# Performance work log

Hardware: AMD Instinct MI355X
Metric: run time of the kernel (lower is better)

The kernel has to match this reference:

```python
import jax, jax.numpy as jnp
import numpy as np
from jax import lax

L_LAYERS = 8
HID = 300


def _reverse_padded(x, lengths):
    # x: [T, B, D]; reverse each sequence within its valid length, keep padding zero.
    T = x.shape[0]
    t = jnp.arange(T)[:, None]                      # [T,1]
    rev = lengths[None, :] - 1 - t                  # [T,B]
    valid = (rev >= 0)
    idx = jnp.clip(rev, 0, T - 1)
    g = jnp.take_along_axis(x, idx[:, :, None].astype(jnp.int32), axis=0)
    return g * valid[:, :, None].astype(x.dtype)


def _run_layer(x, W_ih, W_hh, b, lengths, reverse):
    # x: [T,B,D] time-major. W_ih: [D,6H], W_hh: [H,5H], b: [5H]
    T, B, _ = x.shape
    H = W_hh.shape[0]
    if reverse:
        x = _reverse_padded(x, lengths)
    pi = jnp.einsum('tbd,dg->tbg', x, W_ih)         # [T,B,6H] input projections
    mask = (jnp.arange(T)[:, None] < lengths[None, :])[:, :, None]  # [T,B,1] bool

    def step(carry, xt):
        h, c = carry
        pi_t, m = xt
        ps = h @ W_hh + b                            # [B,5H]
        z = pi_t[:, :5 * H] + ps                     # fused pre-activations
        i = jax.nn.sigmoid(z[:, 0 * H:1 * H])
        f = jax.nn.sigmoid(z[:, 1 * H:2 * H])
        g = jnp.tanh(z[:, 2 * H:3 * H])
        o = jax.nn.sigmoid(z[:, 3 * H:4 * H])
        r = jax.nn.sigmoid(z[:, 4 * H:5 * H])        # highway gate
        c_new = i * g + f * c
        lstm_out = o * jnp.tanh(c_new)
        h_new = r * lstm_out + (1.0 - r) * pi_t[:, 5 * H:]  # highway connection
        c = jnp.where(m, c_new, c)
        h = jnp.where(m, h_new, h)
        return (h, c), h_new * m.astype(h_new.dtype)

    init = (jnp.zeros((B, H), x.dtype), jnp.zeros((B, H), x.dtype))
    (_, _), ys = lax.scan(step, init, (pi, mask))
    if reverse:
        ys = _reverse_padded(ys, lengths)
    return ys


def setup_inputs() -> dict:
    key = jax.random.key(0)
    ks = jax.random.split(key, 6)
    B, T, D = 64, 256, 200
    inputs = jax.random.normal(ks[0], (B, T, D), dtype=jnp.float32)
    lengths = jnp.sort(jax.random.randint(ks[1], (B,), 1, T + 1))[::-1].astype(jnp.int32)
    s = 0.08
    W_ih0 = jax.random.normal(ks[2], (D, 6 * HID), dtype=jnp.float32) * s
    W_ih_rest = jax.random.normal(ks[3], (L_LAYERS - 1, HID, 6 * HID), dtype=jnp.float32) * s
    W_hh = jax.random.normal(ks[4], (L_LAYERS, HID, 5 * HID), dtype=jnp.float32) * s
    b_hh = jnp.zeros((L_LAYERS, 5 * HID), dtype=jnp.float32)
    b_hh = b_hh.at[:, HID:2 * HID].set(1.0)  # forget-gate bias init to 1
    return {"inputs": inputs, "lengths": lengths, "W_ih0": W_ih0,
            "W_ih_rest": W_ih_rest, "W_hh": W_hh, "b_hh": b_hh}


def reference(inputs, lengths, W_ih0, W_ih_rest, W_hh, b_hh):
    # inputs: [B,T,D] batch-first -> time-major [T,B,D]
    x = jnp.transpose(inputs, (1, 0, 2))
    per_layer = []
    for layer in range(L_LAYERS):
        Wih = W_ih0 if layer == 0 else W_ih_rest[layer - 1]
        x = _run_layer(x, Wih, W_hh[layer], b_hh[layer], lengths, reverse=(layer % 2 == 1))
        per_layer.append(x)
    hidden = jnp.stack(per_layer)                    # [L,T,B,H] (matches hy[:,1:])
    output = jnp.transpose(x, (1, 0, 2))             # [B,T,H], zero past lengths
    return output, hidden
```

## Files before the change

### kernel.cpp

```cpp
#include <hip/hip_runtime.h>
#include <hip/hip_bf16.h>

#define B_ 64
#define T_ 256
#define D_ 200
#define H_ 300
#define L_ 8
#define M_ 16384
#define NG 1800
#define NZ 1500
#define KP 320
#define NBP 2048

typedef __attribute__((ext_vector_type(8))) short bf16x8;
typedef __attribute__((ext_vector_type(4))) float f32x4;
typedef __attribute__((ext_vector_type(4))) unsigned u32x4;
typedef unsigned long long ull;

__device__ __forceinline__ unsigned short f2bf(float f) {
  union { float f; unsigned u; } v; v.f = f;
  unsigned r = v.u + 0x7fffu + ((v.u >> 16) & 1u);
  return (unsigned short)(r >> 16);
}

__device__ __forceinline__ float sigf(float x) { return 1.f / (1.f + __expf(-x)); }
__device__ __forceinline__ float tanhf_(float x) {
  x = fminf(15.f, fmaxf(-15.f, x));
  float e = __expf(2.f * x);
  return (e - 1.f) / (e + 1.f);
}

#define BARRIER() asm volatile("s_waitcnt lgkmcnt(0)\n\ts_barrier" ::: "memory")

__device__ __forceinline__ u32x4 ld128_nt(const ull* p) {
  u32x4 v;
  asm volatile("global_load_dwordx4 %0, %1, off nt\n\ts_waitcnt vmcnt(0)"
               : "=v"(v) : "v"(p) : "memory");
  return v;
}
__device__ __forceinline__ u32x4 ld128_sys(const ull* p) {
  u32x4 v;
  asm volatile("global_load_dwordx4 %0, %1, off sc0 sc1\n\ts_waitcnt vmcnt(0)"
               : "=v"(v) : "v"(p) : "memory");
  return v;
}
__device__ __forceinline__ int ld32_nt(const int* p) {
  int v;
  asm volatile("global_load_dword %0, %1, off nt\n\ts_waitcnt vmcnt(0)"
               : "=v"(v) : "v"(p) : "memory");
  return v;
}
__device__ __forceinline__ void st64_plain(ull* p, ull v) {
  asm volatile("global_store_dwordx2 %0, %1, off" :: "v"(p), "v"(v) : "memory");
}
__device__ __forceinline__ void st64_sys(ull* p, ull v) {
  asm volatile("global_store_dwordx2 %0, %1, off sc0 sc1" :: "v"(p), "v"(v) : "memory");
}

__device__ __forceinline__ void gl_lds16(const unsigned short* g, unsigned short* l) {
  __builtin_amdgcn_global_load_lds(
      (const __attribute__((address_space(1))) void*)g,
      (__attribute__((address_space(3))) void*)l, 16, 0, 0);
}

__global__ void k_transpose_w(const float* __restrict__ W0, const float* __restrict__ Wr,
                              unsigned short* __restrict__ WbT) {
  __shared__ unsigned short t_lds[64][65];
  const int n0 = blockIdx.x * 64;
  const int k0 = blockIdx.y * 64;
  const int l = blockIdx.z;
  const int Kl = (l == 0) ? D_ : H_;
  const float* W = (l == 0) ? W0 : (Wr + (size_t)(l - 1) * H_ * NG);
  unsigned short* out = WbT + (size_t)l * NBP * KP;
  const int tx = threadIdx.x & 63;
  const int ty = threadIdx.x >> 6;
  #pragma unroll
  for (int i = 0; i < 16; i++) {
    int k = k0 + ty * 16 + i;
    int n = n0 + tx;
    float v = (k < Kl && n < NG) ? W[(size_t)k * NG + n] : 0.f;
    t_lds[ty * 16 + i][tx] = f2bf(v);
  }
  __syncthreads();
  #pragma unroll
  for (int i = 0; i < 16; i++) {
    int n = n0 + ty * 16 + i;
    if (n < NG) out[(size_t)n * KP + k0 + tx] = t_lds[tx][ty * 16 + i];
  }
}

__global__ void k_transpose_in(const float* __restrict__ inp, unsigned short* __restrict__ xb) {
  int i = blockIdx.x * blockDim.x + threadIdx.x;
  if (i >= T_ * B_ * D_) return;
  int d = i % D_;
  int r = i / D_;
  int b = r % B_;
  int t = r / B_;
  xb[(size_t)r * KP + d] = f2bf(inp[((size_t)b * T_ + t) * D_ + d]);
}

__global__ void k_out(const float* __restrict__ hid7, float* __restrict__ outp) {
  int i = blockIdx.x * blockDim.x + threadIdx.x;
  if (i >= B_ * T_ * H_) return;
  int j = i % H_;
  int r = i / H_;
  int t = r % T_;
  int b = r / T_;
  outp[i] = hid7[((size_t)t * B_ + b) * H_ + j];
}

__global__ __launch_bounds__(256) void k_gemm(const unsigned short* __restrict__ A,
                                              const unsigned short* __restrict__ Bt,
                                              float* __restrict__ C, int nk) {
  __shared__ unsigned short As[128 * 32];
  __shared__ unsigned short Bs[128 * 32];
  const int bm = blockIdx.x, bn = blockIdx.y;
  const int tid = threadIdx.x;
  const int lane = tid & 63, wid = tid >> 6;
  const int wm = wid & 1, wn = wid >> 1;
  const int l16 = lane & 15, quad = lane >> 4;
  const int srow = lane >> 2;
  const int sswz = ((lane & 3) ^ (srow & 3)) << 3;
  const int sA = ((quad ^ (l16 & 3)) << 3);
  const size_t arow0 = (size_t)bm * 128;
  const size_t brow0 = (size_t)bn * 128;
  f32x4 acc[4][4] = {};
  for (int kc = 0; kc < nk; kc++) {
    const int k0 = kc << 5;
    #pragma unroll
    for (int r = 0; r < 2; r++) {
      const int rbase = r * 64 + wid * 16;
      gl_lds16(A  + (arow0 + rbase + srow) * KP + k0 + sswz, &As[rbase * 32]);
      gl_lds16(Bt + (brow0 + rbase + srow) * KP + k0 + sswz, &Bs[rbase * 32]);
    }
    asm volatile("s_waitcnt vmcnt(0)" ::: "memory");
    __syncthreads();
    bf16x8 af[4], bfr[4];
    #pragma unroll
    for (int i = 0; i < 4; i++) {
      af[i]  = *(const bf16x8*)&As[(wm * 64 + i * 16 + l16) * 32 + sA];
      bfr[i] = *(const bf16x8*)&Bs[(wn * 64 + i * 16 + l16) * 32 + sA];
    }
    #pragma unroll
    for (int mi = 0; mi < 4; mi++)
      #pragma unroll
      for (int ni = 0; ni < 4; ni++)
        acc[mi][ni] = __builtin_amdgcn_mfma_f32_16x16x32_bf16(af[mi], bfr[ni], acc[mi][ni], 0, 0, 0);
    __syncthreads();
  }
  const int row0 = bm * 128 + wm * 64 + quad * 4;
  const int col0 = bn * 128 + wn * 64 + l16;
  #pragma unroll
  for (int mi = 0; mi < 4; mi++) {
    #pragma unroll
    for (int ni = 0; ni < 4; ni++) {
      int col = col0 + ni * 16;
      if (col < NG) {
        #pragma unroll
        for (int i = 0; i < 4; i++)
          C[(size_t)(row0 + mi * 16 + i) * NG + col] = acc[mi][ni][i];
      }
    }
  }
}

struct PiR { float v0, v1, v2, v3, v4, v6; };

__device__ __forceinline__ void pi_pref_row(PiR& r, const float* __restrict__ pi,
                                            int lr, int rev, int ss, int br, int j2) {
  r.v0 = r.v1 = r.v2 = r.v3 = r.v4 = r.v6 = 0.f;
  if (ss < lr) {
    int t = rev ? (lr - 1 - ss) : ss;
    const float* pr = pi + ((size_t)t * B_ + br) * NG;
    r.v0 = pr[j2]; r.v1 = pr[300 + j2]; r.v2 = pr[600 + j2];
    r.v3 = pr[900 + j2]; r.v4 = pr[1200 + j2]; r.v6 = pr[NZ + j2];
  }
}

__device__ __forceinline__ void poll_stash(unsigned tg, int par, int pt,
                                           const ull* hwf, const ull* hws,
                                           unsigned short* h_lds) {
  const ull* pf = hwf + par + 2 * pt;
  const ull* ps = hws + par + 2 * pt;
  u32x4 v;
  int miss = 0;
  for (;;) {
    v = ld128_nt(pf);
    if ((v.y == tg) && (v.w == tg)) break;
    if ((++miss & 31) == 0) {
      v = ld128_sys(ps);
      if ((v.y == tg) && (v.w == tg)) break;
      __builtin_amdgcn_s_sleep(1);
    }
  }
  int w0 = pt << 1;
  int r2 = (w0 >= 300) ? 1 : 0;
  int k = w0 - r2 * 300;
  h_lds[(2 * r2) * 328 + k]     = (unsigned short)(v.x >> 16);
  h_lds[(2 * r2 + 1) * 328 + k] = (unsigned short)(v.x & 0xffffu);
  int w1 = w0 + 1;
  int r2b = (w1 >= 300) ? 1 : 0;
  int kb = w1 - r2b * 300;
  h_lds[(2 * r2b) * 328 + kb]     = (unsigned short)(v.z >> 16);
  h_lds[(2 * r2b + 1) * 328 + kb] = (unsigned short)(v.z & 0xffffu);
}

__global__ __launch_bounds__(512, 2) void k_fused(
    float* __restrict__ pi, const float* __restrict__ Whh,
    const float* __restrict__ bias, const int* __restrict__ lens,
    float* __restrict__ hid, unsigned short* __restrict__ xb,
    ull* __restrict__ h_words, int* __restrict__ prog,
    const unsigned short* __restrict__ Bt_next, int rev, int tagbase)
{
  const int bid = blockIdx.x;
  const int tid = threadIdx.x;

  if (bid < 192) {
    __shared__ __align__(16) unsigned short h_lds[16 * 328];
    __shared__ __align__(16) float z_lds[128 * 4];
    __shared__ float bias_s[128];
    __shared__ int len_s[4];

    const int g = bid & 15;
    const int cb = bid >> 4;

    const int lane = tid & 63;
    const int wid = tid >> 6;
    const int l16 = lane & 15;
    const int quad = lane >> 4;

    const int rp = tid / 25;
    const int gj = tid - rp * 25;
    const int j2 = cb * 25 + gj;

    bf16x8 wfrag[10];
    {
      int n = wid * 16 + l16;
      bool vn = n < 125;
      int colw = vn ? ((n / 25) * 300 + cb * 25 + (n % 25)) : 0;
      #pragma unroll
      for (int c = 0; c < 10; c++) {
        bf16x8 f;
        #pragma unroll
        for (int j = 0; j < 8; j++) {
          int k = c * 32 + quad * 8 + j;
          float v = (vn && k < 300) ? Whh[(size_t)k * NZ + colw] : 0.f;
          f[j] = (short)f2bf(v);
        }
        wfrag[c] = f;
      }
    }
    if (tid < 4) len_s[tid] = lens[g * 4 + tid];
    if (tid < 125) bias_s[tid] = bias[(tid / 25) * 300 + cb * 25 + (tid % 25)];
    for (int i = tid; i < 16 * 328; i += 512) h_lds[i] = 0;
    __syncthreads();

    int S = len_s[0];
    S = len_s[1] > S ? len_s[1] : S;
    S = len_s[2] > S ? len_s[2] : S;
    S = len_s[3] > S ? len_s[3] : S;

    ull* hwf = h_words + (size_t)g * 1200;
    ull* hws = h_words + 16 * 1200 + (size_t)g * 1200;
    const int brbase = g * 4;
    float cA = 0.f, cB = 0.f;

    PiR pa, pb;
    int lA = 0, lB = 0;
    if (tid < 50) {
      lA = len_s[2 * rp]; lB = len_s[2 * rp + 1];
      pi_pref_row(pa, pi, lA, rev, 0, brbase + 2 * rp,     j2);
      pi_pref_row(pb, pi, lB, rev, 0, brbase + 2 * rp + 1, j2);
    }

    for (int s = 0; s < S; s++) {
      if (s > 0 && tid >= 64 && tid < 364)
        poll_stash((unsigned)(tagbase + s), (s & 1) * 600, tid - 64, hwf, hws, h_lds);
      BARRIER();

      f32x4 acc = {0, 0, 0, 0};
      if (s > 0) {
        f32x4 acc2 = {0, 0, 0, 0};
        const unsigned short* abase = &h_lds[l16 * 328 + quad * 8];
        #pragma unroll
        for (int c = 0; c < 10; c += 2) {
          bf16x8 a0 = *(const bf16x8*)(abase + c * 32);
          bf16x8 a1 = *(const bf16x8*)(abase + c * 32 + 32);
          acc  = __builtin_amdgcn_mfma_f32_16x16x32_bf16(a0, wfrag[c],     acc,  0, 0, 0);
          acc2 = __builtin_amdgcn_mfma_f32_16x16x32_bf16(a1, wfrag[c + 1], acc2, 0, 0, 0);
        }
        acc += acc2;
      }
      if (quad == 0) {
        int n = wid * 16 + l16;
        *(f32x4*)&z_lds[n * 4] = acc;
      }
      BARRIER();

      if (tid < 50) {
        asm volatile("s_waitcnt vmcnt(0)" ::: "memory");
        const float bb0 = bias_s[gj],      bb1 = bias_s[25 + gj], bb2 = bias_s[50 + gj];
        const float bb3 = bias_s[75 + gj], bb4 = bias_s[100 + gj];
        const float2 z0 = *(const float2*)&z_lds[(gj      ) * 4 + 2 * rp];
        const float2 z1 = *(const float2*)&z_lds[(25 + gj ) * 4 + 2 * rp];
        const float2 z2 = *(const float2*)&z_lds[(50 + gj ) * 4 + 2 * rp];
        const float2 z3 = *(const float2*)&z_lds[(75 + gj ) * 4 + 2 * rp];
        const float2 z4 = *(const float2*)&z_lds[(100 + gj) * 4 + 2 * rp];
        float iA = sigf(z0.x + pa.v0 + bb0);
        float fA = sigf(z1.x + pa.v1 + bb1);
        float gA = tanhf_(z2.x + pa.v2 + bb2);
        float oA = sigf(z3.x + pa.v3 + bb3);
        float rA = sigf(z4.x + pa.v4 + bb4);
        float cnA = iA * gA + fA * cA; cA = cnA;
        float hA = rA * (oA * tanhf_(cnA)) + (1.f - rA) * pa.v6;
        float iB = sigf(z0.y + pb.v0 + bb0);
        float fB = sigf(z1.y + pb.v1 + bb1);
        float gB = tanhf_(z2.y + pb.v2 + bb2);
        float oB = sigf(z3.y + pb.v3 + bb3);
        float rB = sigf(z4.y + pb.v4 + bb4);
        float cnB = iB * gB + fB * cB; cB = cnB;
        float hB = rB * (oB * tanhf_(cnB)) + (1.f - rB) * pb.v6;

        unsigned short hbA = f2bf(hA), hbB = f2bf(hB);
        ull word = ((ull)(unsigned)(tagbase + s + 1) << 32)
                 | ((unsigned)hbA << 16) | (unsigned)hbB;
        int pidx = ((s + 1) & 1) * 600 + rp * 300 + j2;
        st64_plain(hwf + pidx, word);
        st64_sys(hws + pidx, word);
        if (tid == 0) prog[g * 12 + cb] = tagbase + s + 1;
        if (s < lA) {
          int t = rev ? (lA - 1 - s) : s;
          int br = brbase + 2 * rp;
          hid[((size_t)t * B_ + br) * H_ + j2] = hA;
          xb[((size_t)t * B_ + br) * KP + j2] = hbA;
        }
        if (s < lB) {
          int t = rev ? (lB - 1 - s) : s;
          int br = brbase + 2 * rp + 1;
          hid[((size_t)t * B_ + br) * H_ + j2] = hB;
          xb[((size_t)t * B_ + br) * KP + j2] = hbB;
        }
        pi_pref_row(pa, pi, lA, rev, s + 1, brbase + 2 * rp,     j2);
        pi_pref_row(pb, pi, lB, rev, s + 1, brbase + 2 * rp + 1, j2);
      }
    }
    if (tid < 64) {
      asm volatile("s_waitcnt vmcnt(0)" ::: "memory");
      if (tid == 0) prog[g * 12 + cb] = tagbase + 299;
    }
  } else {
    __shared__ unsigned short As[128 * 32];
    __shared__ unsigned short Bs2[2][128 * 32];
    const int w = bid - 192;
    const int cls = w & 7;
    const int k8 = w >> 3;
    const int g = (k8 < 4) ? cls : cls + 8;
    const int q = k8 & 3;
    const int lane = tid & 63;
    const int wid = tid >> 6;
    const int wg = tid >> 8;
    const int w4 = wid & 3;
    const int l16 = lane & 15, quad = lane >> 4;
    const int srow = lane >> 2;
    const int sswz = ((lane & 3) ^ (srow & 3)) << 3;
    const int sA = ((quad ^ (l16 & 3)) << 3);
    const int wm = w4 & 1, wn = w4 >> 1;
    const int Sg = lens[4 * g];

    for (int ci = 0; ci < 8; ci++) {
      const int chunk = rev ? (7 - ci) : ci;
      const int t0 = chunk * 32;
      int need = rev ? (Sg - t0 + 1) : (t0 + 33);
      if (t0 >= Sg) need = 0;
      if (need > 0) {
        if (tid == 0) {
          const int target = tagbase + need;
          for (;;) {
            int mn = 0x7fffffff;
            for (int cbx = 0; cbx < 12; cbx++) {
              int v = ld32_nt(prog + g * 12 + cbx);
              mn = v < mn ? v : mn;
            }
            if (mn >= target) break;
            __builtin_amdgcn_s_sleep(8);
          }
        }
        __syncthreads();
      }
      #pragma unroll 1
      for (int cpi = 0; cpi < 2; cpi++) {
        const int cp = 2 * q + cpi;
        const unsigned short* BtB = Bt_next + (size_t)(cp * 256 + wg * 128) * KP;
        f32x4 acc[4][4] = {};
        for (int kc = 0; kc < 10; kc++) {
          const int k0 = kc << 5;
          {
            int rl = wid * 16 + srow;
            int xrow = (t0 + (rl >> 2)) * 64 + g * 4 + (rl & 3);
            gl_lds16(xb + (size_t)xrow * KP + k0 + sswz, &As[(wid * 16) * 32]);
          }
          #pragma unroll
          for (int r = 0; r < 2; r++) {
            int rbase = w4 * 32 + r * 16;
            gl_lds16(BtB + (size_t)(rbase + srow) * KP + k0 + sswz, &Bs2[wg][rbase * 32]);
          }
          asm volatile("s_waitcnt vmcnt(0)" ::: "memory");
          __syncthreads();
          bf16x8 af[4], bfr[4];
          #pragma unroll
          for (int i = 0; i < 4; i++) {
            af[i]  = *(const bf16x8*)&As[(wm * 64 + i * 16 + l16) * 32 + sA];
            bfr[i] = *(const bf16x8*)&Bs2[wg][(wn * 64 + i * 16 + l16) * 32 + sA];
          }
          #pragma unroll
          for (int mi = 0; mi < 4; mi++)
            #pragma unroll
            for (int ni = 0; ni < 4; ni++)
              acc[mi][ni] = __builtin_amdgcn_mfma_f32_16x16x32_bf16(af[mi], bfr[ni], acc[mi][ni], 0, 0, 0);
          __syncthreads();
        }
        #pragma unroll
        for (int mi = 0; mi < 4; mi++) {
          #pragma unroll
          for (int ni = 0; ni < 4; ni++) {
            int col = cp * 256 + wg * 128 + wn * 64 + ni * 16 + l16;
            if (col < NG) {
              #pragma unroll
              for (int i = 0; i < 4; i++) {
                int rl = wm * 64 + mi * 16 + quad * 4 + i;
                int prow = (t0 + (rl >> 2)) * 64 + g * 4 + (rl & 3);
                pi[(size_t)prow * NG + col] = acc[mi][ni][i];
              }
            }
          }
        }
      }
    }
  }
}

extern "C" void kernel_launch(void* const* d_in, const int* in_sizes, int n_in,
                              void* d_out, int out_size, void* d_ws, size_t ws_size,
                              hipStream_t stream) {
  const float* inputs = (const float*)d_in[0];
  const int* lengths = (const int*)d_in[1];
  const float* W_ih0 = (const float*)d_in[2];
  const float* W_ih_rest = (const float*)d_in[3];
  const float* W_hh = (const float*)d_in[4];
  const float* b_hh = (const float*)d_in[5];
  float* outp = (float*)d_out;
  float* hidden = outp + (size_t)B_ * T_ * H_;

  char* ws = (char*)d_ws;
  float* pi = (float*)ws;
  size_t off = (size_t)M_ * NG * 4;
  unsigned short* xb = (unsigned short*)(ws + off);
  off += (size_t)M_ * KP * 2;
  unsigned short* WbT = (unsigned short*)(ws + off);
  off += (size_t)L_ * NBP * KP * 2;
  ull* h_words = (ull*)(ws + off);
  size_t hw_bytes = 32ull * 1200 * 8 + 16 * 12 * 4;
  int* prog = (int*)(ws + off + 32ull * 1200 * 8);
  off += hw_bytes;

  hipMemsetAsync(d_out, 0, (size_t)out_size * 4, stream);
  hipMemsetAsync(h_words, 0, hw_bytes, stream);
  hipMemsetAsync(xb, 0, (size_t)M_ * KP * 2, stream);
  hipMemsetAsync(WbT, 0, (size_t)L_ * NBP * KP * 2, stream);

  k_transpose_w<<<dim3(29, 5, 8), 256, 0, stream>>>(W_ih0, W_ih_rest, WbT);
  {
    int n = T_ * B_ * D_;
    k_transpose_in<<<(n + 255) / 256, 256, 0, stream>>>(inputs, xb);
  }
  k_gemm<<<dim3(M_ / 128, 15), 256, 0, stream>>>(xb, WbT, pi, 7);
  for (int l = 0; l < L_; l++) {
    float* hid_l = hidden + (size_t)l * T_ * B_ * H_;
    const unsigned short* Bt_next = WbT + (size_t)(l + 1) * NBP * KP;
    int grid = (l < L_ - 1) ? 256 : 192;
    k_fused<<<grid, 512, 0, stream>>>(pi, W_hh + (size_t)l * H_ * NZ, b_hh + (size_t)l * NZ,
                                      lengths, hid_l, xb, h_words, prog,
                                      Bt_next, l & 1, l * 300);
  }
  k_out<<<((B_ * T_ * H_) + 255) / 256, 256, 0, stream>>>(
      hidden + (size_t)(L_ - 1) * T_ * B_ * H_, outp);
}
```

Measured before the change: 3.326 ms.

## Poll per-group epoch counters before reading tagged hidden words

Replaces per-thread polling on tagged hidden-state words with a wave-level ballot over 12 per-column-block epoch counters. Producers publish an epoch after their hidden stores drain, through both plain and system-scope stores. The old tag-polling loop stays as a fallback. Also splits the recurrent MFMA chain into four accumulators, drops the s>0 guard, and raises wave priority in the gate/activation section. The extra waitcnt before publishing the epoch adds latency on the critical path, and correctness now depends on the epoch store becoming visible after the data stores.

```diff
diff --git a/kernel.cpp b/kernel.cpp
--- a/kernel.cpp
+++ b/kernel.cpp
@@ -50,11 +50,23 @@
                : "=v"(v) : "v"(p) : "memory");
   return v;
 }
+__device__ __forceinline__ int ld32_sys_i(const int* p) {
+  int v;
+  asm volatile("global_load_dword %0, %1, off sc0 sc1\n\ts_waitcnt vmcnt(0)"
+               : "=v"(v) : "v"(p) : "memory");
+  return v;
+}
 __device__ __forceinline__ void st64_plain(ull* p, ull v) {
   asm volatile("global_store_dwordx2 %0, %1, off" :: "v"(p), "v"(v) : "memory");
 }
 __device__ __forceinline__ void st64_sys(ull* p, ull v) {
   asm volatile("global_store_dwordx2 %0, %1, off sc0 sc1" :: "v"(p), "v"(v) : "memory");
+}
+__device__ __forceinline__ void st32_plain(int* p, int v) {
+  asm volatile("global_store_dword %0, %1, off" :: "v"(p), "v"(v) : "memory");
+}
+__device__ __forceinline__ void st32_sys_i(int* p, int v) {
+  asm volatile("global_store_dword %0, %1, off sc0 sc1" :: "v"(p), "v"(v) : "memory");
 }
 
 __device__ __forceinline__ void gl_lds16(const unsigned short* g, unsigned short* l) {
@@ -177,39 +189,11 @@
   }
 }
 
-__device__ __forceinline__ void poll_stash(unsigned tg, int par, int pt,
-                                           const ull* hwf, const ull* hws,
-                                           unsigned short* h_lds) {
-  const ull* pf = hwf + par + 2 * pt;
-  const ull* ps = hws + par + 2 * pt;
-  u32x4 v;
-  int miss = 0;
-  for (;;) {
-    v = ld128_nt(pf);
-    if ((v.y == tg) && (v.w == tg)) break;
-    if ((++miss & 31) == 0) {
-      v = ld128_sys(ps);
-      if ((v.y == tg) && (v.w == tg)) break;
-      __builtin_amdgcn_s_sleep(1);
-    }
-  }
-  int w0 = pt << 1;
-  int r2 = (w0 >= 300) ? 1 : 0;
-  int k = w0 - r2 * 300;
-  h_lds[(2 * r2) * 328 + k]     = (unsigned short)(v.x >> 16);
-  h_lds[(2 * r2 + 1) * 328 + k] = (unsigned short)(v.x & 0xffffu);
-  int w1 = w0 + 1;
-  int r2b = (w1 >= 300) ? 1 : 0;
-  int kb = w1 - r2b * 300;
-  h_lds[(2 * r2b) * 328 + kb]     = (unsigned short)(v.z >> 16);
-  h_lds[(2 * r2b + 1) * 328 + kb] = (unsigned short)(v.z & 0xffffu);
-}
-
 __global__ __launch_bounds__(512, 2) void k_fused(
     float* __restrict__ pi, const float* __restrict__ Whh,
     const float* __restrict__ bias, const int* __restrict__ lens,
     float* __restrict__ hid, unsigned short* __restrict__ xb,
-    ull* __restrict__ h_words, int* __restrict__ prog,
+    ull* __restrict__ h_words, int* __restrict__ ep_pl, int* __restrict__ ep_sy,
     const unsigned short* __restrict__ Bt_next, int rev, int tagbase)
 {
   const int bid = blockIdx.x;
@@ -262,6 +246,8 @@
 
     ull* hwf = h_words + (size_t)g * 1200;
     ull* hws = h_words + 16 * 1200 + (size_t)g * 1200;
+    int* epl = ep_pl + g * 16;
+    int* eps = ep_sy + g * 16;
     const int brbase = g * 4;
     float cA = 0.f, cB = 0.f;
 
@@ -274,31 +260,74 @@
     }
 
     for (int s = 0; s < S; s++) {
-      if (s > 0 && tid >= 64 && tid < 364)
-        poll_stash((unsigned)(tagbase + s), (s & 1) * 600, tid - 64, hwf, hws, h_lds);
+      if (s > 0 && tid >= 64 && tid < 364) {
+        const unsigned tg = (unsigned)(tagbase + s);
+        const int par = (s & 1) * 600;
+        const int pt = tid - 64;
+        const ull* pf = hwf + par + 2 * pt;
+        const ull* ps = hws + par + 2 * pt;
+        u32x4 v;
+        bool ok = false;
+        for (int it = 0; it < 64; ++it) {
+          int e = (lane < 12) ? ld32_nt(epl + lane) : 0x7fffffff;
+          ull bal = __ballot(e >= (int)tg);
+          if ((bal & 0xFFFull) == 0xFFFull) { ok = true; break; }
+        }
+        if (ok) {
+          v = ld128_nt(pf);
+          ok = (v.y == tg) && (v.w == tg);
+        }
+        if (!ok) {
+          int miss = 0;
+          for (;;) {
+            v = ld128_nt(pf);
+            if ((v.y == tg) && (v.w == tg)) break;
+            if ((++miss & 31) == 0) {
+              v = ld128_sys(ps);
+              if ((v.y == tg) && (v.w == tg)) break;
+              __builtin_amdgcn_s_sleep(1);
+            }
+          }
+        }
+        int w0 = pt << 1;
+        int r2 = (w0 >= 300) ? 1 : 0;
+        int k = w0 - r2 * 300;
+        h_lds[(2 * r2) * 328 + k]     = (unsigned short)(v.x >> 16);
+        h_lds[(2 * r2 + 1) * 328 + k] = (unsigned short)(v.x & 0xffffu);
+        int w1 = w0 + 1;
+        int r2b = (w1 >= 300) ? 1 : 0;
+        int kb = w1 - r2b * 300;
+        h_lds[(2 * r2b) * 328 + kb]     = (unsigned short)(v.z >> 16);
+        h_lds[(2 * r2b + 1) * 328 + kb] = (unsigned short)(v.z & 0xffffu);
+      }
       BARRIER();
 
-      f32x4 acc = {0, 0, 0, 0};
-      if (s > 0) {
-        f32x4 acc2 = {0, 0, 0, 0};
+      {
+        f32x4 a0 = {0,0,0,0}, a1 = {0,0,0,0}, a2 = {0,0,0,0}, a3 = {0,0,0,0};
         const unsigned short* abase = &h_lds[l16 * 328 + quad * 8];
         #pragma unroll
-        for (int c = 0; c < 10; c += 2) {
-          bf16x8 a0 = *(const bf16x8*)(abase + c * 32);
-          bf16x8 a1 = *(const bf16x8*)(abase + c * 32 + 32);
-          acc  = __builtin_amdgcn_mfma_f32_16x16x32_bf16(a0, wfrag[c],     acc,  0, 0, 0);
-          acc2 = __builtin_amdgcn_mfma_f32_16x16x32_bf16(a1, wfrag[c + 1], acc2, 0, 0, 0);
-        }
-        acc += acc2;
-      }
-      if (quad == 0) {
-        int n = wid * 16 + l16;
-        *(f32x4*)&z_lds[n * 4] = acc;
+        for (int c = 0; c < 10; c += 4) {
+          bf16x8 h0 = *(const bf16x8*)(abase + c * 32);
+          bf16x8 h1 = *(const bf16x8*)(abase + c * 32 + 32);
+          a0 = __builtin_amdgcn_mfma_f32_16x16x32_bf16(h0, wfrag[c],     a0, 0, 0, 0);
+          a1 = __builtin_amdgcn_mfma_f32_16x16x32_bf16(h1, wfrag[c + 1], a1, 0, 0, 0);
+          if (c + 2 < 10) {
+            bf16x8 h2 = *(const bf16x8*)(abase + c * 32 + 64);
+            bf16x8 h3 = *(const bf16x8*)(abase + c * 32 + 96);
+            a2 = __builtin_amdgcn_mfma_f32_16x16x32_bf16(h2, wfrag[c + 2], a2, 0, 0, 0);
+            a3 = __builtin_amdgcn_mfma_f32_16x16x32_bf16(h3, wfrag[c + 3], a3, 0, 0, 0);
+          }
+        }
+        f32x4 acc = (a0 + a1) + (a2 + a3);
+        if (quad == 0) {
+          int n = wid * 16 + l16;
+          *(f32x4*)&z_lds[n * 4] = acc;
+        }
       }
       BARRIER();
 
       if (tid < 50) {
-        asm volatile("s_waitcnt vmcnt(0)" ::: "memory");
+        __builtin_amdgcn_s_setprio(1);
         const float bb0 = bias_s[gj],      bb1 = bias_s[25 + gj], bb2 = bias_s[50 + gj];
         const float bb3 = bias_s[75 + gj], bb4 = bias_s[100 + gj];
         const float2 z0 = *(const float2*)&z_lds[(gj      ) * 4 + 2 * rp];
@@ -326,8 +355,12 @@
                  | ((unsigned)hbA << 16) | (unsigned)hbB;
         int pidx = ((s + 1) & 1) * 600 + rp * 300 + j2;
         st64_plain(hwf + pidx, word);
+        asm volatile("s_waitcnt vmcnt(0)" ::: "memory");
+        if (tid == 0) {
+          st32_plain(epl + cb, tagbase + s + 1);
+          st32_sys_i(eps + cb, tagbase + s + 1);
+        }
         st64_sys(hws + pidx, word);
-        if (tid == 0) prog[g * 12 + cb] = tagbase + s + 1;
         if (s < lA) {
           int t = rev ? (lA - 1 - s) : s;
           int br = brbase + 2 * rp;
@@ -342,11 +375,13 @@
         }
         pi_pref_row(pa, pi, lA, rev, s + 1, brbase + 2 * rp,     j2);
         pi_pref_row(pb, pi, lB, rev, s + 1, brbase + 2 * rp + 1, j2);
-      }
-    }
-    if (tid < 64) {
+        __builtin_amdgcn_s_setprio(0);
+      }
+    }
+    if (tid == 0) {
       asm volatile("s_waitcnt vmcnt(0)" ::: "memory");
-      if (tid == 0) prog[g * 12 + cb] = tagbase + 299;
+      st32_plain(epl + cb, tagbase + 299);
+      st32_sys_i(eps + cb, tagbase + 299);
     }
   } else {
     __shared__ unsigned short As[128 * 32];
@@ -375,13 +410,16 @@
       if (need > 0) {
         if (tid == 0) {
           const int target = tagbase + need;
+          int iters = 0;
           for (;;) {
             int mn = 0x7fffffff;
             for (int cbx = 0; cbx < 12; cbx++) {
-              int v = ld32_nt(prog + g * 12 + cbx);
+              int v = (iters < 256) ? ld32_nt(ep_pl + g * 16 + cbx)
+                                    : ld32_sys_i(ep_sy + g * 16 + cbx);
               mn = v < mn ? v : mn;
             }
             if (mn >= target) break;
+            iters++;
             __builtin_amdgcn_s_sleep(8);
           }
         }
@@ -459,8 +497,10 @@
   unsigned short* WbT = (unsigned short*)(ws + off);
   off += (size_t)L_ * NBP * KP * 2;
   ull* h_words = (ull*)(ws + off);
-  size_t hw_bytes = 32ull * 1200 * 8 + 16 * 12 * 4;
-  int* prog = (int*)(ws + off + 32ull * 1200 * 8);
+  size_t data_bytes = 32ull * 1200 * 8;
+  int* ep_pl = (int*)(ws + off + data_bytes);
+  int* ep_sy = ep_pl + 16 * 16;
+  size_t hw_bytes = data_bytes + 2ull * 16 * 16 * 4;
   off += hw_bytes;
 
   hipMemsetAsync(d_out, 0, (size_t)out_size * 4, stream);
@@ -479,7 +519,7 @@
     const unsigned short* Bt_next = WbT + (size_t)(l + 1) * NBP * KP;
     int grid = (l < L_ - 1) ? 256 : 192;
     k_fused<<<grid, 512, 0, stream>>>(pi, W_hh + (size_t)l * H_ * NZ, b_hh + (size_t)l * NZ,
-                                      lengths, hid_l, xb, h_words, prog,
+                                      lengths, hid_l, xb, h_words, ep_pl, ep_sy,
                                       Bt_next, l & 1, l * 300);
   }
   k_out<<<((B_ * T_ * H_) + 255) / 256, 256, 0, stream>>>(
```

New measurement: 3.799 ms. +14.2%, slower.

## Split recurrent gate math across two waves, one batch row per lane

Applied to the files above, without the earlier changes.

The per-step LSTM/highway gate evaluation is spread from 50 threads handling two batch rows each to 100 lanes across two waves handling one row each. A lane shuffle then packs the two bf16 results into the tagged exchange word. The h-polling threads shift to make room. Gate lanes raise their scheduling priority while they run, and the recurrent MFMA chain uses four independent accumulators instead of two. The aim is to shorten the serial per-timestep critical path, at the cost of an extra shuffle and more waves taking part in the gate phase.

```diff
diff --git a/kernel.cpp b/kernel.cpp
--- a/kernel.cpp
+++ b/kernel.cpp
@@ -166,8 +166,8 @@
 
 struct PiR { float v0, v1, v2, v3, v4, v6; };
 
-__device__ __forceinline__ void pi_pref_row(PiR& r, const float* __restrict__ pi,
-                                            int lr, int rev, int ss, int br, int j2) {
+__device__ __forceinline__ void pi_pref6(PiR& r, const float* __restrict__ pi,
+                                         int lr, int rev, int ss, int br, int j2) {
   r.v0 = r.v1 = r.v2 = r.v3 = r.v4 = r.v6 = 0.f;
   if (ss < lr) {
     int t = rev ? (lr - 1 - ss) : ss;
@@ -229,9 +229,11 @@
     const int l16 = lane & 15;
     const int quad = lane >> 4;
 
-    const int rp = tid / 25;
-    const int gj = tid - rp * 25;
-    const int j2 = cb * 25 + gj;
+    const int gw = wid;
+    const bool is_gate = (gw < 2) && (lane < 50);
+    const int grow = gw * 2 + (lane >= 25 ? 1 : 0);
+    const int gcol = (lane >= 25) ? lane - 25 : lane;
+    const int j2 = cb * 25 + gcol;
 
     bf16x8 wfrag[10];
     {
@@ -263,90 +265,94 @@
     ull* hwf = h_words + (size_t)g * 1200;
     ull* hws = h_words + 16 * 1200 + (size_t)g * 1200;
     const int brbase = g * 4;
-    float cA = 0.f, cB = 0.f;
-
-    PiR pa, pb;
-    int lA = 0, lB = 0;
-    if (tid < 50) {
-      lA = len_s[2 * rp]; lB = len_s[2 * rp + 1];
-      pi_pref_row(pa, pi, lA, rev, 0, brbase + 2 * rp,     j2);
-      pi_pref_row(pb, pi, lB, rev, 0, brbase + 2 * rp + 1, j2);
+    float cr = 0.f;
+
+    PiR pa;
+    int lr = 0;
+    if (is_gate) {
+      lr = len_s[grow];
+      pi_pref6(pa, pi, lr, rev, 0, brbase + grow, j2);
     }
 
     for (int s = 0; s < S; s++) {
-      if (s > 0 && tid >= 64 && tid < 364)
-        poll_stash((unsigned)(tagbase + s), (s & 1) * 600, tid - 64, hwf, hws, h_lds);
+      if (s > 0) {
+        if (tid >= 128 && tid < 428)
+          poll_stash((unsigned)(tagbase + s), (s & 1) * 600, tid - 128, hwf, hws, h_lds);
+        else if (tid >= 64 && tid < 128)
+          asm volatile("s_waitcnt vmcnt(0)" ::: "memory");
+      }
       BARRIER();
 
-      f32x4 acc = {0, 0, 0, 0};
-      if (s > 0) {
-        f32x4 acc2 = {0, 0, 0, 0};
-        const unsigned short* abase = &h_lds[l16 * 328 + quad * 8];
-        #pragma unroll
-        for (int c = 0; c < 10; c += 2) {
-          bf16x8 a0 = *(const bf16x8*)(abase + c * 32);
-          bf16x8 a1 = *(const bf16x8*)(abase + c * 32 + 32);
-          acc  = __builtin_amdgcn_mfma_f32_16x16x32_bf16(a0, wfrag[c],     acc,  0, 0, 0);
-          acc2 = __builtin_amdgcn_mfma_f32_16x16x32_bf16(a1, wfrag[c + 1], acc2, 0, 0, 0);
-        }
-        acc += acc2;
-      }
-      if (quad == 0) {
-        int n = wid * 16 + l16;
-        *(f32x4*)&z_lds[n * 4] = acc;
+      {
+        f32x4 a0 = {0,0,0,0}, a1 = {0,0,0,0}, a2 = {0,0,0,0}, a3 = {0,0,0,0};
+        if (s > 0) {
+          const unsigned short* abase = &h_lds[l16 * 328 + quad * 8];
+          #pragma unroll
+          for (int c = 0; c < 10; c += 4) {
+            bf16x8 h0 = *(const bf16x8*)(abase + c * 32);
+            bf16x8 h1 = *(const bf16x8*)(abase + c * 32 + 32);
+            a0 = __builtin_amdgcn_mfma_f32_16x16x32_bf16(h0, wfrag[c],     a0, 0, 0, 0);
+            a1 = __builtin_amdgcn_mfma_f32_16x16x32_bf16(h1, wfrag[c + 1], a1, 0, 0, 0);
+            if (c + 2 < 10) {
+              bf16x8 h2 = *(const bf16x8*)(abase + c * 32 + 64);
+              bf16x8 h3 = *(const bf16x8*)(abase + c * 32 + 96);
+              a2 = __builtin_amdgcn_mfma_f32_16x16x32_bf16(h2, wfrag[c + 2], a2, 0, 0, 0);
+              a3 = __builtin_amdgcn_mfma_f32_16x16x32_bf16(h3, wfrag[c + 3], a3, 0, 0, 0);
+            }
+          }
+        }
+        f32x4 acc = (a0 + a1) + (a2 + a3);
+        if (quad == 0) {
+          int n = wid * 16 + l16;
+          *(f32x4*)&z_lds[n * 4] = acc;
+        }
       }
       BARRIER();
 
-      if (tid < 50) {
+      if (is_gate) {
+        __builtin_amdgcn_s_setprio(1);
         asm volatile("s_waitcnt vmcnt(0)" ::: "memory");
-        const float bb0 = bias_s[gj],      bb1 = bias_s[25 + gj], bb2 = bias_s[50 + gj];
-        const float bb3 = bias_s[75 + gj], bb4 = bias_s[100 + gj];
-        const float2 z0 = *(const float2*)&z_lds[(gj      ) * 4 + 2 * rp];
-        const float2 z1 = *(const float2*)&z_lds[(25 + gj ) * 4 + 2 * rp];
-        const float2 z2 = *(const float2*)&z_lds[(50 + gj ) * 4 + 2 * rp];
-        const float2 z3 = *(const float2*)&z_lds[(75 + gj ) * 4 + 2 * rp];
-        const float2 z4 = *(const float2*)&z_lds[(100 + gj) * 4 + 2 * rp];
-        float iA = sigf(z0.x + pa.v0 + bb0);
-        float fA = sigf(z1.x + pa.v1 + bb1);
-        float gA = tanhf_(z2.x + pa.v2 + bb2);
-        float oA = sigf(z3.x + pa.v3 + bb3);
-        float rA = sigf(z4.x + pa.v4 + bb4);
-        float cnA = iA * gA + fA * cA; cA = cnA;
-        float hA = rA * (oA * tanhf_(cnA)) + (1.f - rA) * pa.v6;
-        float iB = sigf(z0.y + pb.v0 + bb0);
-        float fB = sigf(z1.y + pb.v1 + bb1);
-        float gB = tanhf_(z2.y + pb.v2 + bb2);
-        float oB = sigf(z3.y + pb.v3 + bb3);
-        float rB = sigf(z4.y + pb.v4 + bb4);
-        float cnB = iB * gB + fB * cB; cB = cnB;
-        float hB = rB * (oB * tanhf_(cnB)) + (1.f - rB) * pb.v6;
-
-        unsigned short hbA = f2bf(hA), hbB = f2bf(hB);
-        ull word = ((ull)(unsigned)(tagbase + s + 1) << 32)
-                 | ((unsigned)hbA << 16) | (unsigned)hbB;
-        int pidx = ((s + 1) & 1) * 600 + rp * 300 + j2;
-        st64_plain(hwf + pidx, word);
-        st64_sys(hws + pidx, word);
+        const float bb0 = bias_s[gcol],      bb1 = bias_s[25 + gcol];
+        const float bb2 = bias_s[50 + gcol], bb3 = bias_s[75 + gcol];
+        const float bb4 = bias_s[100 + gcol];
+        float z0 = z_lds[(gcol      ) * 4 + grow];
+        float z1 = z_lds[(25 + gcol ) * 4 + grow];
+        float z2 = z_lds[(50 + gcol ) * 4 + grow];
+        float z3 = z_lds[(75 + gcol ) * 4 + grow];
+        float z4 = z_lds[(100 + gcol) * 4 + grow];
+        float ii = sigf(z0 + pa.v0 + bb0);
+        float ff = sigf(z1 + pa.v1 + bb1);
+        float gg = tanhf_(z2 + pa.v2 + bb2);
+        float oo = sigf(z3 + pa.v3 + bb3);
+        float rr = sigf(z4 + pa.v4 + bb4);
+        float cn = ii * gg + ff * cr; cr = cn;
+        float h = rr * (oo * tanhf_(cn)) + (1.f - rr) * pa.v6;
+        unsigned short hb = f2bf(h);
+        unsigned hbO = (unsigned)__shfl((int)(unsigned)hb, lane + 25);
+        if (lane < 25) {
+          ull word = ((ull)(unsigned)(tagbase + s + 1) << 32)
+                   | ((unsigned)hb << 16) | (hbO & 0xffffu);
+          int pidx = ((s + 1) & 1) * 600 + gw * 300 + j2;
+          st64_plain(hwf + pidx, word);
+          st64_sys(hws + pidx, word);
+        }
         if (tid == 0) prog[g * 12 + cb] = tagbase + s + 1;
-        if (s < lA) {
-          int t = rev ? (lA - 1 - s) : s;
-          int br = brbase + 2 * rp;
-          hid[((size_t)t * B_ + br) * H_ + j2] = hA;
-          xb[((size_t)t * B_ + br) * KP + j2] = hbA;
-        }
-        if (s < lB) {
-          int t = rev ? (lB - 1 - s) : s;
-          int br = brbase + 2 * rp + 1;
-          hid[((size_t)t * B_ + br) * H_ + j2] = hB;
-          xb[((size_t)t * B_ + br) * KP + j2] = hbB;
-        }
-        pi_pref_row(pa, pi, lA, rev, s + 1, brbase + 2 * rp,     j2);
-        pi_pref_row(pb, pi, lB, rev, s + 1, brbase + 2 * rp + 1, j2);
-      }
-    }
-    if (tid < 64) {
+        if (s < lr) {
+          int t = rev ? (lr - 1 - s) : s;
+          int br = brbase + grow;
+          hid[((size_t)t * B_ + br) * H_ + j2] = h;
+          xb[((size_t)t * B_ + br) * KP + j2] = hb;
+        }
+        pi_pref6(pa, pi, lr, rev, s + 1, brbase + grow, j2);
+        __builtin_amdgcn_s_setprio(0);
+      }
+    }
+    if (tid >= 64 && tid < 128)
       asm volatile("s_waitcnt vmcnt(0)" ::: "memory");
-      if (tid == 0) prog[g * 12 + cb] = tagbase + 299;
+    __syncthreads();
+    if (tid == 0) {
+      asm volatile("s_waitcnt vmcnt(0)" ::: "memory");
+      prog[g * 12 + cb] = tagbase + 299;
     }
   } else {
     __shared__ unsigned short As[128 * 32];
@@ -459,8 +465,9 @@
   unsigned short* WbT = (unsigned short*)(ws + off);
   off += (size_t)L_ * NBP * KP * 2;
   ull* h_words = (ull*)(ws + off);
-  size_t hw_bytes = 32ull * 1200 * 8 + 16 * 12 * 4;
-  int* prog = (int*)(ws + off + 32ull * 1200 * 8);
+  size_t data_bytes = 32ull * 1200 * 8;
+  int* prog = (int*)(ws + off + data_bytes);
+  size_t hw_bytes = data_bytes + 16ull * 12 * 4;
   off += hw_bytes;
 
   hipMemsetAsync(d_out, 0, (size_t)out_size * 4, stream);
```

Measured after the change: 3.220 ms. 1.03x faster.
